# Performance work log

Measured on AMD Instinct MI355X. Metric: run time of the kernel, lower is better.

The kernel has to match this reference:

```python
import jax, jax.numpy as jnp
import numpy as np

B, T, D, H = 256, 1024, 128, 128

def setup_inputs() -> dict:
    key = jax.random.key(0)
    k1, k2, k3, k4 = jax.random.split(key, 4)
    return {
        "x": jax.random.normal(k1, (B, T, D), dtype=jnp.float32),
        "w": jax.random.normal(k2, (D, H), dtype=jnp.float32) * 0.05,
        "state_weight": jax.random.normal(k3, (H, H), dtype=jnp.float32) * 0.05,
        "b": jax.random.normal(k4, (H,), dtype=jnp.float32) * 0.05,
    }

def reference(x, w, state_weight, b):
    # Faithful Elman RNN with return_sequences=False.
    # Original transposes input to time-major [T, B, D], initializes the
    # state from step 0 WITHOUT a recurrent term, then iterates steps 1..T-1.
    X = jnp.transpose(x, (1, 0, 2))  # [T, B, D]
    # Precompute input projections for all steps in one big GEMM (same math).
    proj = jnp.einsum("tbd,dh->tbh", X, w) + b  # [T, B, H]
    state0 = jnp.tanh(proj[0])

    def step(state, pt):
        y = jnp.tanh(pt + state @ state_weight)
        return y, None

    final_state, _ = jax.lax.scan(step, state0, proj[1:])
    return final_state  # [B, H]
```

## Files before the change

kernel.cpp:

```cpp
#include <hip/hip_runtime.h>

#define T_N 1024
#define H_N 128
#define CH   64
#define NCH (T_N / CH)
#define WPAD 136
#define PPAD 68

typedef __attribute__((ext_vector_type(8))) short bf16x8;
typedef __attribute__((ext_vector_type(4))) float f32x4;

__device__ __forceinline__ short f2bf_rne(float f) {
    union { float f; unsigned int i; } v; v.f = f;
    unsigned int r = v.i + 0x7FFFu + ((v.i >> 16) & 1u);
    return (short)(r >> 16);
}
__device__ __forceinline__ float tanh_fast(float x) {
    return 1.0f - 2.0f / (__expf(2.0f * x) + 1.0f);
}

__global__ __launch_bounds__(512, 1) void k_fused(const float* __restrict__ x,
                                                  const float* __restrict__ w,
                                                  const float* __restrict__ wst,
                                                  const float* __restrict__ bias,
                                                  float* __restrict__ out) {
    __shared__ __align__(16) short wT[H_N * WPAD];
    __shared__ __align__(16) float pT[H_N * PPAD];
    __shared__ __align__(16) short sst[2][H_N];

    const int tid  = threadIdx.x;
    const int wv   = tid >> 6;
    const int lane = tid & 63;
    const int l = lane & 15;
    const int q = lane >> 4;
    const int tt = wv >> 1;
    const int h  = wv & 1;
    const int r = blockIdx.x;
    const float* xrow = x + (size_t)r * T_N * H_N;
    const f32x4 zero4 = (f32x4){0.f, 0.f, 0.f, 0.f};

    const float* xlane = xrow + (size_t)(tt * 16 + l) * H_N + q * 8;
    float4 xst[8];
    #pragma unroll
    for (int ks = 0; ks < 4; ++ks) {
        xst[ks * 2 + 0] = *reinterpret_cast<const float4*>(xlane + ks * 32);
        xst[ks * 2 + 1] = *reinterpret_cast<const float4*>(xlane + ks * 32 + 4);
    }

    short* wsTs = reinterpret_cast<short*>(pT);
    for (int e = tid * 4; e < H_N * H_N; e += 2048) {
        int k = e >> 7, n = e & 127;
        float4 a4 = *reinterpret_cast<const float4*>(wst + e);
        wsTs[(n + 0) * WPAD + k] = f2bf_rne(a4.x);
        wsTs[(n + 1) * WPAD + k] = f2bf_rne(a4.y);
        wsTs[(n + 2) * WPAD + k] = f2bf_rne(a4.z);
        wsTs[(n + 3) * WPAD + k] = f2bf_rne(a4.w);
    }
    __syncthreads();

    bf16x8 wf[4];
    #pragma unroll
    for (int ks = 0; ks < 4; ++ks)
        wf[ks] = *reinterpret_cast<const bf16x8*>(
            &wsTs[(16 * wv + l) * WPAD + ks * 32 + q * 8]);
    __syncthreads();

    for (int e = tid * 4; e < H_N * H_N; e += 2048) {
        int k = e >> 7, n = e & 127;
        float4 a4 = *reinterpret_cast<const float4*>(w + e);
        wT[(n + 0) * WPAD + k] = f2bf_rne(a4.x);
        wT[(n + 1) * WPAD + k] = f2bf_rne(a4.y);
        wT[(n + 2) * WPAD + k] = f2bf_rne(a4.z);
        wT[(n + 3) * WPAD + k] = f2bf_rne(a4.w);
    }

    float bv[4];
    #pragma unroll
    for (int j = 0; j < 4; ++j) bv[j] = bias[(4 * h + j) * 16 + l];

    int par = 0;
    float y = 0.f;
    const int rowp = (16 * wv + l) * PPAD;

    #pragma unroll 1
    for (int c = 0; c < NCH; ++c) {
        bf16x8 ax[4];
        #pragma unroll
        for (int ks = 0; ks < 4; ++ks) {
            float4 u0 = xst[ks * 2 + 0];
            float4 u1 = xst[ks * 2 + 1];
            bf16x8 f;
            f[0] = f2bf_rne(u0.x); f[1] = f2bf_rne(u0.y);
            f[2] = f2bf_rne(u0.z); f[3] = f2bf_rne(u0.w);
            f[4] = f2bf_rne(u1.x); f[5] = f2bf_rne(u1.y);
            f[6] = f2bf_rne(u1.z); f[7] = f2bf_rne(u1.w);
            ax[ks] = f;
        }

        if (c + 1 < NCH) {
            const float* pn = xlane + (size_t)(c + 1) * CH * H_N;
            #pragma unroll
            for (int ks = 0; ks < 4; ++ks) {
                xst[ks * 2 + 0] = *reinterpret_cast<const float4*>(pn + ks * 32);
                xst[ks * 2 + 1] = *reinterpret_cast<const float4*>(pn + ks * 32 + 4);
            }
        }

        __syncthreads();

        #pragma unroll
        for (int j = 0; j < 4; ++j) {
            const int nt = 4 * h + j;
            f32x4 acc;
            #pragma unroll
            for (int ks = 0; ks < 4; ++ks) {
                bf16x8 bw = *reinterpret_cast<const bf16x8*>(
                    &wT[(nt * 16 + l) * WPAD + ks * 32 + q * 8]);
                acc = __builtin_amdgcn_mfma_f32_16x16x32_bf16(
                    ax[ks], bw, ks == 0 ? zero4 : acc, 0, 0, 0);
            }
            f32x4 o = (f32x4){acc[0] + bv[j], acc[1] + bv[j],
                              acc[2] + bv[j], acc[3] + bv[j]};
            *reinterpret_cast<f32x4*>(&pT[(nt * 16 + l) * PPAD + tt * 16 + q * 4]) = o;
        }

        __syncthreads();

        int tstart = 0;
        if (c == 0) {
            if (tid < 128)
                sst[0][tid] = f2bf_rne(tanh_fast(pT[tid * PPAD + 0]));
            __syncthreads();
            tstart = 1;
            par = 0;
        }

        float p = pT[rowp + tstart];

        #pragma unroll 1
        for (int t = tstart; t < CH; ++t) {
            bf16x8 a[4];
            #pragma unroll
            for (int ks = 0; ks < 4; ++ks)
                a[ks] = *reinterpret_cast<const bf16x8*>(&sst[par][ks * 32 + q * 8]);

            f32x4 acc[4];
            #pragma unroll
            for (int ks = 0; ks < 4; ++ks)
                acc[ks] = __builtin_amdgcn_mfma_f32_16x16x32_bf16(
                    a[ks], wf[ks], zero4, 0, 0, 0);

            int tn = (t + 1 < CH) ? t + 1 : t;
            float np = pT[rowp + tn];

            float z = p + ((acc[0][0] + acc[1][0]) + (acc[2][0] + acc[3][0]));
            y = tanh_fast(z);
            if (q == 0)
                sst[par ^ 1][16 * wv + l] = f2bf_rne(y);
            p = np;
            par ^= 1;
            __syncthreads();
        }
    }

    if (q == 0)
        out[r * H_N + 16 * wv + l] = y;
}

extern "C" void kernel_launch(void* const* d_in, const int* in_sizes, int n_in,
                              void* d_out, int out_size, void* d_ws, size_t ws_size,
                              hipStream_t stream) {
    const float* x    = (const float*)d_in[0];
    const float* w    = (const float*)d_in[1];
    const float* wst  = (const float*)d_in[2];
    const float* bias = (const float*)d_in[3];
    float* out = (float*)d_out;

    k_fused<<<256, 512, 0, stream>>>(x, w, wst, bias, out);
}
```

Before: 448.3 us.

## Streamline recurrent step: zero-init state, fold bias/proj into MFMA accumulators, unroll by two

Removes the special first-step path by starting from a zero state, which is equivalent because tanh(p0 + 0·W) equals the original initialisation. Bias and the per-step input projection are now passed in as the MFMA accumulator input instead of being added afterwards. The tanh uses a hardware reciprocal and the bf16 conversion uses the packed convert instruction. The time loop is unrolled by two with fixed ping-pong buffers, and one redundant barrier per chunk is dropped. The serial per-step critical path gets shorter, with slightly lower tanh precision as the trade.

Result: faster. 375.2 us (-16.3%).

```diff
diff --git a/kernel.cpp b/kernel.cpp
--- a/kernel.cpp
+++ b/kernel.cpp
@@ -14,9 +14,6 @@
     union { float f; unsigned int i; } v; v.f = f;
     unsigned int r = v.i + 0x7FFFu + ((v.i >> 16) & 1u);
     return (short)(r >> 16);
-}
-__device__ __forceinline__ float tanh_fast(float x) {
-    return 1.0f - 2.0f / (__expf(2.0f * x) + 1.0f);
 }
 
 __global__ __launch_bounds__(512, 1) void k_fused(const float* __restrict__ x,
@@ -63,7 +60,8 @@
     for (int ks = 0; ks < 4; ++ks)
         wf[ks] = *reinterpret_cast<const bf16x8*>(
             &wsTs[(16 * wv + l) * WPAD + ks * 32 + q * 8]);
-    __syncthreads();
+
+    if (tid < 128) sst[0][tid] = 0;
 
     for (int e = tid * 4; e < H_N * H_N; e += 2048) {
         int k = e >> 7, n = e & 127;
@@ -78,9 +76,34 @@
     #pragma unroll
     for (int j = 0; j < 4; ++j) bv[j] = bias[(4 * h + j) * 16 + l];
 
-    int par = 0;
+    __syncthreads();
+
     float y = 0.f;
+    float p = 0.f;
     const int rowp = (16 * wv + l) * PPAD;
+
+    auto step = [&](const short* srd, short* swr, int t) {
+        bf16x8 a0 = *reinterpret_cast<const bf16x8*>(&srd[ 0 + q * 8]);
+        bf16x8 a1 = *reinterpret_cast<const bf16x8*>(&srd[32 + q * 8]);
+        bf16x8 a2 = *reinterpret_cast<const bf16x8*>(&srd[64 + q * 8]);
+        bf16x8 a3 = *reinterpret_cast<const bf16x8*>(&srd[96 + q * 8]);
+        int tn = (t + 1 < CH) ? t + 1 : t;
+        float np = pT[rowp + tn];
+        f32x4 c4 = (f32x4){p, p, p, p};
+        f32x4 x0 = __builtin_amdgcn_mfma_f32_16x16x32_bf16(a0, wf[0], c4, 0, 0, 0);
+        f32x4 x1 = __builtin_amdgcn_mfma_f32_16x16x32_bf16(a1, wf[1], zero4, 0, 0, 0);
+        f32x4 x2 = __builtin_amdgcn_mfma_f32_16x16x32_bf16(a2, wf[2], zero4, 0, 0, 0);
+        f32x4 x3 = __builtin_amdgcn_mfma_f32_16x16x32_bf16(a3, wf[3], zero4, 0, 0, 0);
+        float z = (x0[0] + x1[0]) + (x2[0] + x3[0]);
+        float e = __expf(2.0f * z);
+        y = __builtin_fmaf(-2.0f, __builtin_amdgcn_rcpf(e + 1.0f), 1.0f);
+        unsigned int pk;
+        asm("v_cvt_pk_bf16_f32 %0, %1, %2" : "=v"(pk) : "v"(y), "v"(y));
+        if (q == 0)
+            swr[16 * wv + l] = (short)pk;
+        p = np;
+        __syncthreads();
+    };
 
     #pragma unroll 1
     for (int c = 0; c < NCH; ++c) {
@@ -106,60 +129,30 @@
             }
         }
 
-        __syncthreads();
 
         #pragma unroll
         for (int j = 0; j < 4; ++j) {
             const int nt = 4 * h + j;
+            f32x4 cb = (f32x4){bv[j], bv[j], bv[j], bv[j]};
             f32x4 acc;
             #pragma unroll
             for (int ks = 0; ks < 4; ++ks) {
                 bf16x8 bw = *reinterpret_cast<const bf16x8*>(
                     &wT[(nt * 16 + l) * WPAD + ks * 32 + q * 8]);
                 acc = __builtin_amdgcn_mfma_f32_16x16x32_bf16(
-                    ax[ks], bw, ks == 0 ? zero4 : acc, 0, 0, 0);
+                    ax[ks], bw, ks == 0 ? cb : acc, 0, 0, 0);
             }
-            f32x4 o = (f32x4){acc[0] + bv[j], acc[1] + bv[j],
-                              acc[2] + bv[j], acc[3] + bv[j]};
-            *reinterpret_cast<f32x4*>(&pT[(nt * 16 + l) * PPAD + tt * 16 + q * 4]) = o;
+            *reinterpret_cast<f32x4*>(&pT[(nt * 16 + l) * PPAD + tt * 16 + q * 4]) = acc;
         }
 
         __syncthreads();
 
-        int tstart = 0;
-        if (c == 0) {
-            if (tid < 128)
-                sst[0][tid] = f2bf_rne(tanh_fast(pT[tid * PPAD + 0]));
-            __syncthreads();
-            tstart = 1;
-            par = 0;
-        }
-
-        float p = pT[rowp + tstart];
+        p = pT[rowp];
 
         #pragma unroll 1
-        for (int t = tstart; t < CH; ++t) {
-            bf16x8 a[4];
-            #pragma unroll
-            for (int ks = 0; ks < 4; ++ks)
-                a[ks] = *reinterpret_cast<const bf16x8*>(&sst[par][ks * 32 + q * 8]);
-
-            f32x4 acc[4];
-            #pragma unroll
-            for (int ks = 0; ks < 4; ++ks)
-                acc[ks] = __builtin_amdgcn_mfma_f32_16x16x32_bf16(
-                    a[ks], wf[ks], zero4, 0, 0, 0);
-
-            int tn = (t + 1 < CH) ? t + 1 : t;
-            float np = pT[rowp + tn];
-
-            float z = p + ((acc[0][0] + acc[1][0]) + (acc[2][0] + acc[3][0]));
-            y = tanh_fast(z);
-            if (q == 0)
-                sst[par ^ 1][16 * wv + l] = f2bf_rne(y);
-            p = np;
-            par ^= 1;
-            __syncthreads();
+        for (int t = 0; t < CH; t += 2) {
+            step(sst[0], sst[1], t);
+            step(sst[1], sst[0], t + 1);
         }
     }
 
```
